# Kernel optimization log

Hardware: AMD Instinct MI355X
Metric: run time of the kernel (lower is better)

Reference implementation:

```python
import jax, jax.numpy as jnp
import numpy as np

B, S, HID = 1, 2048, 2304
H, KV, D = 8, 4, 256
FF = 9216
CAP = 50.0                      # attn_logit_softcapping
SCALE = 256.0 ** -0.5           # query_pre_attn_scalar ** -0.5
WIN = 1024                      # sliding_window_size
EPS = 1e-6
NEG = -2.3819763e38


def setup_inputs() -> dict:
    key = jax.random.key(0)
    ks = jax.random.split(key, 11)
    w = lambda k, shp: jax.random.normal(k, shp, jnp.float32) * 0.02
    ln = lambda k: jax.random.normal(k, (HID,), jnp.float32) * 0.1
    hidden_states = jax.random.normal(ks[0], (B, S, HID), jnp.float32)
    qkv_w = w(ks[1], (HID, (H + 2 * KV) * D))
    o_w = w(ks[2], (H * D, HID))
    gate_w = w(ks[3], (HID, FF))
    up_w = w(ks[4], (HID, FF))
    down_w = w(ks[5], (FF, HID))
    in_ln_w = ln(ks[6]); post_attn_ln_w = ln(ks[7])
    pre_ffw_ln_w = ln(ks[8]); post_ffw_ln_w = ln(ks[9])
    # precompute_freqs_cis (theta=10000) as cos/sin of shape [S, D//2]
    inv = 1.0 / (10000.0 ** (np.arange(0, D, 2)[: D // 2].astype(np.float64) / D))
    fr = np.outer(np.arange(S), inv)
    cos = jnp.asarray(np.cos(fr), jnp.float32)
    sin = jnp.asarray(np.sin(fr), jnp.float32)
    kv_write_indices = jnp.arange(S, dtype=jnp.int32)
    k_cache = jnp.zeros((B, S, KV, D), jnp.float32)
    v_cache = jnp.zeros((B, S, KV, D), jnp.float32)
    causal = jnp.tril(jnp.ones((S, S), bool))
    mask = jnp.where(causal, 0.0, NEG).astype(jnp.float32)[None, None]
    return dict(hidden_states=hidden_states, qkv_w=qkv_w, o_w=o_w,
                gate_w=gate_w, up_w=up_w, down_w=down_w,
                in_ln_w=in_ln_w, post_attn_ln_w=post_attn_ln_w,
                pre_ffw_ln_w=pre_ffw_ln_w, post_ffw_ln_w=post_ffw_ln_w,
                cos=cos, sin=sin, kv_write_indices=kv_write_indices,
                k_cache=k_cache, v_cache=v_cache, mask=mask)


def rmsnorm(x, wt):
    x = x.astype(jnp.float32)
    x = x * jax.lax.rsqrt(jnp.mean(x * x, axis=-1, keepdims=True) + EPS)
    return x * (1.0 + wt)  # add_unit_offset=True


def rope(x, cos, sin):
    # x: [b,s,h,d]; complex rotation with real=first half, imag=second half
    x1, x2 = jnp.split(x, 2, axis=-1)
    c = cos[None, :, None, :]
    s = sin[None, :, None, :]
    return jnp.concatenate([x1 * c - x2 * s, x1 * s + x2 * c], axis=-1)


def reference(hidden_states, qkv_w, o_w, gate_w, up_w, down_w,
              in_ln_w, post_attn_ln_w, pre_ffw_ln_w, post_ffw_ln_w,
              cos, sin, kv_write_indices, k_cache, v_cache, mask):
    residual = hidden_states
    x = rmsnorm(hidden_states, in_ln_w)
    qkv = x @ qkv_w
    q = qkv[..., : H * D].reshape(B, S, H, D)
    k = qkv[..., H * D: H * D + KV * D].reshape(B, S, KV, D)
    v = qkv[..., H * D + KV * D:].reshape(B, S, KV, D)
    q = rope(q, cos, sin)
    k = rope(k, cos, sin)
    kc = k_cache.at[:, kv_write_indices].set(k)
    vc = v_cache.at[:, kv_write_indices].set(v)
    g = H // KV
    kr = jnp.repeat(kc, g, axis=2)   # GQA repeat_interleave -> [B,S,H,D]
    vr = jnp.repeat(vc, g, axis=2)
    scores = jnp.einsum('bqhd,bkhd->bhqk', q * SCALE, kr)
    pos = jnp.arange(S)
    band = jnp.abs(pos[:, None] - pos[None, :]) <= (WIN - 1)
    m = jnp.where(band[None, None], mask, NEG)
    scores = jnp.tanh(scores / CAP) * CAP + m
    probs = jax.nn.softmax(scores.astype(jnp.float32), axis=-1)
    attn = jnp.einsum('bhqk,bkhd->bqhd', probs, vr).reshape(B, S, H * D)
    attn = attn @ o_w
    h = residual + rmsnorm(attn, post_attn_ln_w)
    residual = h
    x = rmsnorm(h, pre_ffw_ln_w)
    x = jax.nn.gelu(x @ gate_w, approximate=True) * (x @ up_w)
    x = x @ down_w
    x = rmsnorm(x, post_ffw_ln_w)
    return residual + x
```

## Files before the change

kernel.cpp:

```cpp
#include <hip/hip_runtime.h>
#include <hip/hip_bf16.h>
#include <cstdint>
#include <cstddef>

#define S_LEN  2048
#define HIDDEN 2304
#define NHEAD  8
#define NKVH   4
#define DHEAD  256
#define FFDIM  9216
#define QKVN   4096
#define ODIM   2048
#define WINM1  1023
#define QSCALE 0.0625f
#define CAPF   50.0f
#define PSTR   ((size_t)S_LEN * HIDDEN)

typedef __attribute__((ext_vector_type(4))) float f32x4;
typedef __attribute__((ext_vector_type(8))) short s16x8;

__device__ __forceinline__ void gload_lds16(const void* gptr, void* lptr) {
  __builtin_amdgcn_global_load_lds(
      (const __attribute__((address_space(1))) unsigned int*)gptr,
      (__attribute__((address_space(3))) unsigned int*)lptr, 16, 0, 0);
}

__global__ void k_fill(float* p, float v, size_t n) {
  size_t i = (size_t)blockIdx.x * blockDim.x + threadIdx.x;
  size_t st = (size_t)gridDim.x * blockDim.x;
  for (; i < n; i += st) p[i] = v;
}

__global__ void k_transpose_bf16(const float* __restrict__ in, __hip_bfloat16* __restrict__ out,
                                 int R, int C) {
  __shared__ float tile[32][33];
  const int c0 = blockIdx.x * 32, r0 = blockIdx.y * 32;
  const int tc = threadIdx.x & 31, tr = threadIdx.x >> 5;
#pragma unroll
  for (int i = 0; i < 4; i++)
    tile[tr + 8 * i][tc] = in[(size_t)(r0 + tr + 8 * i) * C + c0 + tc];
  __syncthreads();
#pragma unroll
  for (int i = 0; i < 4; i++)
    out[(size_t)(c0 + tr + 8 * i) * R + r0 + tc] = __float2bfloat16(tile[tc][tr + 8 * i]);
}

template <int NP, bool INBF16, bool ADD, bool BF16OUT>
__global__ void k_rmsnorm(const void* __restrict__ xv, const float* __restrict__ w,
                          const float* __restrict__ res, void* __restrict__ outv) {
  const int row = blockIdx.x;
  __shared__ float xs[HIDDEN];
  float ss = 0.f;
  for (int i = threadIdx.x; i < HIDDEN; i += 256) {
    float v = 0.f;
#pragma unroll
    for (int p = 0; p < NP; p++) {
      if constexpr (INBF16)
        v += __bfloat162float(((const __hip_bfloat16*)xv)[(size_t)p * PSTR + (size_t)row * HIDDEN + i]);
      else
        v += ((const float*)xv)[(size_t)p * PSTR + (size_t)row * HIDDEN + i];
    }
    xs[i] = v;
    ss += v * v;
  }
#pragma unroll
  for (int off = 32; off >= 1; off >>= 1) ss += __shfl_down(ss, off);
  __shared__ float red[4];
  __shared__ float srstd;
  if ((threadIdx.x & 63) == 0) red[threadIdx.x >> 6] = ss;
  __syncthreads();
  if (threadIdx.x == 0) {
    float tot = red[0] + red[1] + red[2] + red[3];
    srstd = rsqrtf(tot / (float)HIDDEN + 1e-6f);
  }
  __syncthreads();
  const float rstd = srstd;
  for (int i = threadIdx.x; i < HIDDEN; i += 256) {
    float v = xs[i] * rstd * (1.f + w[i]);
    if constexpr (ADD) v += res[(size_t)row * HIDDEN + i];
    if constexpr (BF16OUT)
      ((__hip_bfloat16*)outv)[(size_t)row * HIDDEN + i] = __float2bfloat16(v);
    else
      ((float*)outv)[(size_t)row * HIDDEN + i] = v;
  }
}

__global__ void k_rmsnorm2(const float* __restrict__ planes, const float* __restrict__ w1,
                           const float* __restrict__ res, const float* __restrict__ w2,
                           float* __restrict__ hf, __hip_bfloat16* __restrict__ xb) {
  const int row = blockIdx.x;
  __shared__ float xs[HIDDEN];
  __shared__ float red[4];
  __shared__ float srstd;
  float ss = 0.f;
  for (int i = threadIdx.x; i < HIDDEN; i += 256) {
    const float v = planes[(size_t)row * HIDDEN + i] + planes[PSTR + (size_t)row * HIDDEN + i];
    xs[i] = v;
    ss += v * v;
  }
#pragma unroll
  for (int off = 32; off >= 1; off >>= 1) ss += __shfl_down(ss, off);
  if ((threadIdx.x & 63) == 0) red[threadIdx.x >> 6] = ss;
  __syncthreads();
  if (threadIdx.x == 0)
    srstd = rsqrtf((red[0] + red[1] + red[2] + red[3]) / (float)HIDDEN + 1e-6f);
  __syncthreads();
  const float rstd1 = srstd;
  float ss2 = 0.f;
  for (int i = threadIdx.x; i < HIDDEN; i += 256) {
    const float h = res[(size_t)row * HIDDEN + i] + xs[i] * rstd1 * (1.f + w1[i]);
    hf[(size_t)row * HIDDEN + i] = h;
    ss2 += h * h;
  }
  __syncthreads();
  for (int i = threadIdx.x; i < HIDDEN; i += 256)
    xs[i] = hf[(size_t)row * HIDDEN + i];
#pragma unroll
  for (int off = 32; off >= 1; off >>= 1) ss2 += __shfl_down(ss2, off);
  if ((threadIdx.x & 63) == 0) red[threadIdx.x >> 6] = ss2;
  __syncthreads();
  if (threadIdx.x == 0)
    srstd = rsqrtf((red[0] + red[1] + red[2] + red[3]) / (float)HIDDEN + 1e-6f);
  __syncthreads();
  const float rstd2 = srstd;
  for (int i = threadIdx.x; i < HIDDEN; i += 256)
    xb[(size_t)row * HIDDEN + i] = __float2bfloat16(xs[i] * rstd2 * (1.f + w2[i]));
}

template <int EPI>
__global__ __launch_bounds__(256) void k_gemm_bt(const __hip_bfloat16* __restrict__ A,
                                                 const __hip_bfloat16* __restrict__ Bt,
                                                 void* __restrict__ Cv,
                                                 const __hip_bfloat16* __restrict__ G,
                                                 int N, int K) {
  __shared__ alignas(16) __hip_bfloat16 sA[128 * 64];
  __shared__ alignas(16) __hip_bfloat16 sB[128 * 64];
  const int t = threadIdx.x;
  const int w = t >> 6;
  const int wm = w >> 1, wn = w & 1;
  const int nwg = gridDim.x * gridDim.y;
  const int fblk = blockIdx.y * gridDim.x + blockIdx.x;
  const int qq = nwg >> 3, r8 = nwg & 7;
  const int xcd = fblk & 7, ix = fblk >> 3;
  const int swz = (xcd < r8 ? xcd * (qq + 1) : r8 * (qq + 1) + (xcd - r8) * qq) + ix;
  const int m0 = (swz % gridDim.y) * 128, n0 = (swz / gridDim.y) * 128;
  const int lr = t & 15, lg = (t & 63) >> 4;
  const int srow = t >> 3, sc8 = t & 7;

  f32x4 acc[4][4];
#pragma unroll
  for (int a = 0; a < 4; a++)
#pragma unroll
    for (int b = 0; b < 4; b++) acc[a][b] = (f32x4){0.f, 0.f, 0.f, 0.f};

  for (int kt = 0; kt < K; kt += 64) {
#pragma unroll
    for (int i = 0; i < 4; i++) {
      const __hip_bfloat16* g = A + (size_t)(m0 + i * 32 + srow) * K + kt + sc8 * 8;
      gload_lds16(g, sA + (size_t)(i * 256 + w * 64) * 8);
    }
#pragma unroll
    for (int i = 0; i < 4; i++) {
      const __hip_bfloat16* g = Bt + (size_t)(n0 + i * 32 + srow) * K + kt + sc8 * 8;
      gload_lds16(g, sB + (size_t)(i * 256 + w * 64) * 8);
    }
    __syncthreads();
#pragma unroll
    for (int ks = 0; ks < 2; ks++) {
      s16x8 af[4], bfr[4];
#pragma unroll
      for (int fm = 0; fm < 4; fm++)
        af[fm] = *reinterpret_cast<const s16x8*>(sA + (wm * 64 + fm * 16 + lr) * 64 + ks * 32 + lg * 8);
#pragma unroll
      for (int fn = 0; fn < 4; fn++)
        bfr[fn] = *reinterpret_cast<const s16x8*>(sB + (wn * 64 + fn * 16 + lr) * 64 + ks * 32 + lg * 8);
#pragma unroll
      for (int fm = 0; fm < 4; fm++)
#pragma unroll
        for (int fn = 0; fn < 4; fn++)
          acc[fm][fn] = __builtin_amdgcn_mfma_f32_16x16x32_bf16(af[fm], bfr[fn], acc[fm][fn], 0, 0, 0);
    }
    __syncthreads();
  }
#pragma unroll
  for (int fm = 0; fm < 4; fm++) {
    const int rb = m0 + wm * 64 + fm * 16 + lg * 4;
#pragma unroll
    for (int fn = 0; fn < 4; fn++) {
      const int col = n0 + wn * 64 + fn * 16 + lr;
#pragma unroll
      for (int j = 0; j < 4; j++) {
        const size_t idx = (size_t)(rb + j) * N + col;
        if constexpr (EPI == 0) {
          ((float*)Cv)[idx] = acc[fm][fn][j];
        } else if constexpr (EPI == 1) {
          ((__hip_bfloat16*)Cv)[idx] = __float2bfloat16(acc[fm][fn][j]);
        } else {
          const float x = __bfloat162float(G[idx]);
          const float tt = tanhf(0.7978845608028654f * (x + 0.044715f * x * x * x));
          ((__hip_bfloat16*)Cv)[idx] = __float2bfloat16(0.5f * x * (1.f + tt) * acc[fm][fn][j]);
        }
      }
    }
  }
}

template <int EPI>
__global__ __launch_bounds__(512, 2) void k_gemm8(const __hip_bfloat16* __restrict__ A,
                                                  const __hip_bfloat16* __restrict__ Bt,
                                                  void* __restrict__ Cv,
                                                  const __hip_bfloat16* __restrict__ G,
                                                  const __hip_bfloat16* __restrict__ Bt2,
                                                  void* __restrict__ Cv2,
                                                  int N, int K, int keff) {
  __shared__ alignas(16) __hip_bfloat16 smem[65536];
  const int t = threadIdx.x;
  const int w = t >> 6;
  const int wm = w >> 2, wn = w & 3;
  const int l = t & 63;
  const int lr = l & 15, lg = l >> 4;

  const int nxy = gridDim.x * gridDim.y;
  const int nwg = nxy * gridDim.z;
  const int fblk = blockIdx.z * nxy + blockIdx.y * gridDim.x + blockIdx.x;
  const int qq = nwg >> 3, r8 = nwg & 7;
  const int xcd = fblk & 7, ix = fblk >> 3;
  const int swz = (xcd < r8 ? xcd * (qq + 1) : r8 * (qq + 1) + (xcd - r8) * qq) + ix;
  const int plane = swz / nxy;
  const int rem = swz % nxy;
  const int m0 = (rem % gridDim.y) * 256, n0 = (rem / gridDim.y) * 256;
  const int k0 = plane * keff;

  const __hip_bfloat16* Bsrc = Bt;
  int nb0 = n0;
  if constexpr (EPI == 3) {
    if (n0 >= FFDIM) { Bsrc = Bt2; nb0 = n0 - FFDIM; }
  }

  const int sA8 = l & 7;
  size_t aoff[2], boff[2];
#pragma unroll
  for (int j = 0; j < 2; j++) {
    const int rv = (w * 2 + j) * 8 + (l >> 3);
    const int ko = (sA8 ^ (rv & 7)) * 8;
    aoff[j] = (size_t)(m0 + ((rv >> 6) & 1) * 128 + ((rv >> 4) & 3) * 16 + (rv & 15)) * K + k0 + ko;
    boff[j] = (size_t)(nb0 + ((rv >> 5) & 3) * 64 + ((rv >> 4) & 1) * 16 + (rv & 15)) * K + k0 + ko;
  }
  const int sl0 = ((lg) ^ (lr & 7)) * 8;
  const int sl1 = ((4 + lg) ^ (lr & 7)) * 8;

  f32x4 acc[8][4];
#pragma unroll
  for (int a = 0; a < 8; a++)
#pragma unroll
    for (int b = 0; b < 4; b++) acc[a][b] = (f32x4){0.f, 0.f, 0.f, 0.f};
  s16x8 af[4][2], bfr[2][2][2];

#define STG_A(bu, h, kti) { _Pragma("unroll") for (int j = 0; j < 2; j++) \
    gload_lds16(A + aoff[j] + (size_t)(h) * 64 * K + (size_t)(kti) * 64, \
                smem + (bu) * 32768 + (h) * 8192 + (w * 2 + j) * 512); }
#define STG_B(bu, h, kti) { _Pragma("unroll") for (int j = 0; j < 2; j++) \
    gload_lds16(Bsrc + boff[j] + (size_t)(h) * 32 * K + (size_t)(kti) * 64, \
                smem + (bu) * 32768 + 16384 + (h) * 8192 + (w * 2 + j) * 512); }
#define RD_A(bu, fmh) { const __hip_bfloat16* ab_ = smem + (bu) * 32768; \
    _Pragma("unroll") for (int f2 = 0; f2 < 4; f2++) { \
      const int ro_ = ((fmh) * 128 + wm * 64 + f2 * 16 + lr) * 64; \
      af[f2][0] = *(const s16x8*)(ab_ + ro_ + sl0); \
      af[f2][1] = *(const s16x8*)(ab_ + ro_ + sl1); } }
#define RD_BH(bu, fnh) { const __hip_bfloat16* bb_ = smem + (bu) * 32768 + 16384; \
    _Pragma("unroll") for (int f2 = 0; f2 < 2; f2++) { \
      const int ro_ = ((fnh) * 128 + wn * 32 + f2 * 16 + lr) * 64; \
      bfr[fnh][f2][0] = *(const s16x8*)(bb_ + ro_ + sl0); \
      bfr[fnh][f2][1] = *(const s16x8*)(bb_ + ro_ + sl1); } }
#define MFMA16(fmh, fnh) { __builtin_amdgcn_s_setprio(1); \
    _Pragma("unroll") for (int f2 = 0; f2 < 4; f2++) \
    _Pragma("unroll") for (int g2 = 0; g2 < 2; g2++) \
    _Pragma("unroll") for (int ks = 0; ks < 2; ks++) \
      acc[(fmh) * 4 + f2][(fnh) * 2 + g2] = __builtin_amdgcn_mfma_f32_16x16x32_bf16( \
          af[f2][ks], bfr[fnh][g2][ks], acc[(fmh) * 4 + f2][(fnh) * 2 + g2], 0, 0, 0); \
    __builtin_amdgcn_s_setprio(0); }
#define BARR() asm volatile("s_barrier" ::: "memory")
#define LGKM0() asm volatile("s_waitcnt lgkmcnt(0)" ::: "memory")
#define VMC4() asm volatile("s_waitcnt vmcnt(4)" ::: "memory")
#define VMC0() asm volatile("s_waitcnt vmcnt(0)" ::: "memory")

  STG_A(0, 0, 0); STG_A(0, 1, 0); STG_B(0, 0, 0); STG_B(0, 1, 0);
  STG_A(1, 0, 1); STG_A(1, 1, 1);
  VMC4(); BARR();

  const int niter = keff >> 7;
  for (int i = 0; i < niter; ++i) {
    const int t1 = 2 * i + 1;
    const bool more = (i + 1 < niter);
    RD_A(0, 0); RD_BH(0, 0);
    STG_B(1, 0, t1);
    BARR(); LGKM0(); MFMA16(0, 0); BARR();
    RD_BH(0, 1);
    STG_B(1, 1, t1);
    if (more) STG_A(0, 0, t1 + 1);
    BARR(); LGKM0(); MFMA16(0, 1); BARR();
    RD_A(0, 1);
    BARR(); LGKM0(); MFMA16(1, 0); BARR();
    if (more) STG_A(0, 1, t1 + 1);
    BARR(); LGKM0(); MFMA16(1, 1);
    if (more) { VMC4(); } else { VMC0(); }
    BARR();
    RD_A(1, 0); RD_BH(1, 0);
    if (more) STG_B(0, 0, t1 + 1);
    BARR(); LGKM0(); MFMA16(0, 0); BARR();
    RD_BH(1, 1);
    if (more) STG_B(0, 1, t1 + 1);
    BARR(); LGKM0(); MFMA16(0, 1); BARR();
    RD_A(1, 1);
    if (more) STG_A(1, 0, t1 + 2);
    BARR(); LGKM0(); MFMA16(1, 0); BARR();
    if (more) STG_A(1, 1, t1 + 2);
    BARR(); LGKM0(); MFMA16(1, 1);
    if (more) { VMC4(); }
    BARR();
  }
#undef STG_A
#undef STG_B
#undef RD_A
#undef RD_BH
#undef MFMA16
#undef BARR
#undef LGKM0
#undef VMC4
#undef VMC0

  __hip_bfloat16* Cw = nullptr;
  int cbase = n0, cstride = N;
  if constexpr (EPI == 3) {
    Cw = (__hip_bfloat16*)((n0 < FFDIM) ? Cv : Cv2);
    cbase = (n0 < FFDIM) ? n0 : n0 - FFDIM;
    cstride = FFDIM;
  }
#pragma unroll
  for (int fm = 0; fm < 8; fm++) {
    const int rb = m0 + wm * 128 + fm * 16 + lg * 4;
#pragma unroll
    for (int fn = 0; fn < 4; fn++) {
      const int coln = wn * 64 + fn * 16 + lr;
#pragma unroll
      for (int j = 0; j < 4; j++) {
        if constexpr (EPI == 3) {
          Cw[(size_t)(rb + j) * cstride + cbase + coln] = __float2bfloat16(acc[fm][fn][j]);
        } else {
          const size_t idxo = (size_t)(rb + j) * N + n0 + coln;
          if constexpr (EPI == 0) {
            ((float*)Cv)[idxo] = acc[fm][fn][j];
          } else if constexpr (EPI == 1) {
            ((__hip_bfloat16*)Cv)[idxo] = __float2bfloat16(acc[fm][fn][j]);
          } else if constexpr (EPI == 2) {
            const float x = __bfloat162float(G[idxo]);
            const float tg = tanhf(0.7978845608028654f * (x + 0.044715f * x * x * x));
            ((__hip_bfloat16*)Cv)[idxo] = __float2bfloat16(0.5f * x * (1.f + tg) * acc[fm][fn][j]);
          } else if constexpr (EPI == 4) {
            float* P = (plane == 0) ? (float*)Cv : (float*)Cv2;
            P[idxo] = acc[fm][fn][j];
          } else {
            ((__hip_bfloat16*)Cv)[(size_t)plane * PSTR + idxo] = __float2bfloat16(acc[fm][fn][j]);
          }
        }
      }
    }
  }
}

__global__ void k_gelu_mul2(const __hip_bfloat16* __restrict__ g, const __hip_bfloat16* __restrict__ u,
                            __hip_bfloat16* __restrict__ o, int n8) {
  const int st = gridDim.x * blockDim.x;
  for (int i = blockIdx.x * blockDim.x + threadIdx.x; i < n8; i += st) {
    s16x8 gv = *(const s16x8*)(g + (size_t)i * 8);
    s16x8 uv = *(const s16x8*)(u + (size_t)i * 8);
    s16x8 ov;
#pragma unroll
    for (int j = 0; j < 8; j++) {
      const float x = __uint_as_float(((uint32_t)(uint16_t)gv[j]) << 16);
      const float uu = __uint_as_float(((uint32_t)(uint16_t)uv[j]) << 16);
      const float tt = tanhf(0.7978845608028654f * (x + 0.044715f * x * x * x));
      const float r = 0.5f * x * (1.f + tt) * uu;
      ov[j] = (short)(__hip_bfloat16_raw(__float2bfloat16(r)).x);
    }
    *(s16x8*)(o + (size_t)i * 8) = ov;
  }
}

__global__ void k_rope_split(const float* __restrict__ p0, const float* __restrict__ p1,
                             const float* __restrict__ cosb, const float* __restrict__ sinb,
                             __hip_bfloat16* __restrict__ qo, __hip_bfloat16* __restrict__ ko) {
  const int s = blockIdx.x;
  const float* r0 = p0 + (size_t)s * QKVN;
  const float* r1 = p1 + (size_t)s * QKVN;
  const float* cr = cosb + (size_t)s * 128;
  const float* sr = sinb + (size_t)s * 128;
  for (int idx = threadIdx.x; idx < (NHEAD + NKVH) * 128; idx += 256) {
    const int hh = idx >> 7, d = idx & 127;
    const float cv = cr[d], sv = sr[d];
    if (hh < NHEAD) {
      const float x1 = r0[hh * DHEAD + d] + r1[hh * DHEAD + d];
      const float x2 = r0[hh * DHEAD + 128 + d] + r1[hh * DHEAD + 128 + d];
      const size_t base = ((size_t)hh * S_LEN + s) * DHEAD;
      qo[base + d]       = __float2bfloat16((x1 * cv - x2 * sv) * QSCALE);
      qo[base + 128 + d] = __float2bfloat16((x1 * sv + x2 * cv) * QSCALE);
    } else {
      const int kv = hh - NHEAD;
      const int o1 = NHEAD * DHEAD + kv * DHEAD + d;
      const float x1 = r0[o1] + r1[o1];
      const float x2 = r0[o1 + 128] + r1[o1 + 128];
      const size_t base = ((size_t)kv * S_LEN + s) * DHEAD;
      ko[base + d]       = __float2bfloat16(x1 * cv - x2 * sv);
      ko[base + 128 + d] = __float2bfloat16(x1 * sv + x2 * cv);
    }
  }
}

__global__ __launch_bounds__(256) void k_vsplit_t(const float* __restrict__ p0,
                                                  const float* __restrict__ p1,
                                                  __hip_bfloat16* __restrict__ vt) {
  __shared__ float tile[64][260];
  const int s0 = blockIdx.x * 64, kv = blockIdx.y;
  const int t = threadIdx.x;
  const int rr = t >> 6, c4 = t & 63;
#pragma unroll
  for (int p = 0; p < 16; p++) {
    const int row = rr + p * 4;
    const size_t go = (size_t)(s0 + row) * QKVN + (NHEAD + NKVH) * DHEAD + kv * DHEAD + c4 * 4;
    const float4 v0 = *(const float4*)(p0 + go);
    const float4 v1 = *(const float4*)(p1 + go);
    float4 v;
    v.x = v0.x + v1.x; v.y = v0.y + v1.y; v.z = v0.z + v1.z; v.w = v0.w + v1.w;
    *(float4*)(&tile[row][c4 * 4]) = v;
  }
  __syncthreads();
  const int c = t & 31, dr = t >> 5;
#pragma unroll
  for (int p = 0; p < 32; p++) {
    const int d = dr + p * 8;
    __hip_bfloat162 pr;
    pr.x = __float2bfloat16(tile[2 * c][d]);
    pr.y = __float2bfloat16(tile[2 * c + 1][d]);
    *(__hip_bfloat162*)(vt + ((size_t)kv * DHEAD + d) * S_LEN + s0 + 2 * c) = pr;
  }
}

__global__ __launch_bounds__(256) void k_attn_mfma(const __hip_bfloat16* __restrict__ Q,
                                                   const __hip_bfloat16* __restrict__ Kb,
                                                   const __hip_bfloat16* __restrict__ Vt,
                                                   __hip_bfloat16* __restrict__ O) {
  __shared__ alignas(16) __hip_bfloat16 Ks[64 * 264];
  __shared__ alignas(16) __hip_bfloat16 Vs[256 * 72];
  __shared__ alignas(16) __hip_bfloat16 Ps[64 * 72];
  const int h = blockIdx.y, kvh = h >> 1;
  const int q0 = blockIdx.x * 64;
  const int t = threadIdx.x;
  const int wq = t >> 6;
  const int l = t & 63;
  const int lr = l & 15, lg = l >> 4;

  s16x8 qf[8];
  {
    const __hip_bfloat16* qrow = Q + ((size_t)h * S_LEN + q0 + wq * 16 + lr) * DHEAD;
#pragma unroll
    for (int ks = 0; ks < 8; ks++) qf[ks] = *(const s16x8*)(qrow + ks * 32 + lg * 8);
  }
  f32x4 acc[16];
#pragma unroll
  for (int i = 0; i < 16; i++) acc[i] = (f32x4){0.f, 0.f, 0.f, 0.f};
  float rsum[4] = {0.f, 0.f, 0.f, 0.f};

  int lo = q0 - WINM1;
  if (lo < 0) lo = 0;
  lo &= ~63;
  const int qrow_base = q0 + wq * 16 + lg * 4;

  for (int kc = lo; kc <= q0; kc += 64) {
#pragma unroll
    for (int p = 0; p < 8; p++) {
      const int idx = t + p * 256;
      const int row = idx >> 5, c16 = idx & 31;
      s16x8 v = *(const s16x8*)(Kb + ((size_t)kvh * S_LEN + kc + row) * DHEAD + c16 * 8);
      *(s16x8*)(Ks + row * 264 + c16 * 8) = v;
    }
#pragma unroll
    for (int p = 0; p < 8; p++) {
      const int idx = t + p * 256;
      const int d = idx >> 3, ch = idx & 7;
      s16x8 v = *(const s16x8*)(Vt + ((size_t)kvh * DHEAD + d) * S_LEN + kc + ch * 8);
      *(s16x8*)(Vs + d * 72 + ch * 8) = v;
    }
    __syncthreads();

    f32x4 sc[4];
#pragma unroll
    for (int fq = 0; fq < 4; fq++) {
      sc[fq] = (f32x4){0.f, 0.f, 0.f, 0.f};
#pragma unroll
      for (int ks = 0; ks < 8; ks++) {
        s16x8 bfr = *(const s16x8*)(Ks + (fq * 16 + lr) * 264 + ks * 32 + lg * 8);
        sc[fq] = __builtin_amdgcn_mfma_f32_16x16x32_bf16(qf[ks], bfr, sc[fq], 0, 0, 0);
      }
    }
#pragma unroll
    for (int fq = 0; fq < 4; fq++) {
      const int k = kc + fq * 16 + lr;
#pragma unroll
      for (int j = 0; j < 4; j++) {
        const int qw = qrow_base + j;
        float p = 0.f;
        if (k <= qw && qw - k <= WINM1) {
          const float s = sc[fq][j];
          const float u = exp2f(s * 0.057707801635558534f);
          const float arg = 72.134752044448169f -
                            144.26950408889634f * __builtin_amdgcn_rcpf(u + 1.f);
          p = exp2f(arg);
        }
        const __hip_bfloat16 pb = __float2bfloat16(p);
        Ps[(wq * 16 + lg * 4 + j) * 72 + fq * 16 + lr] = pb;
        rsum[j] += __bfloat162float(pb);
      }
    }
#pragma unroll
    for (int ks2 = 0; ks2 < 2; ks2++) {
      s16x8 pa = *(const s16x8*)(Ps + (wq * 16 + lr) * 72 + ks2 * 32 + lg * 8);
#pragma unroll
      for (int f2 = 0; f2 < 16; f2++) {
        s16x8 vb = *(const s16x8*)(Vs + (f2 * 16 + lr) * 72 + ks2 * 32 + lg * 8);
        acc[f2] = __builtin_amdgcn_mfma_f32_16x16x32_bf16(pa, vb, acc[f2], 0, 0, 0);
      }
    }
    __syncthreads();
  }
#pragma unroll
  for (int j = 0; j < 4; j++) {
    float s = rsum[j];
#pragma unroll
    for (int off = 1; off < 16; off <<= 1) s += __shfl_xor(s, off, 64);
    rsum[j] = 1.f / s;
  }
#pragma unroll
  for (int f2 = 0; f2 < 16; f2++)
#pragma unroll
    for (int j = 0; j < 4; j++)
      O[(size_t)(qrow_base + j) * ODIM + h * DHEAD + f2 * 16 + lr] =
          __float2bfloat16(acc[f2][j] * rsum[j]);
}

extern "C" void kernel_launch(void* const* d_in, const int* in_sizes, int n_in,
                              void* d_out, int out_size, void* d_ws, size_t ws_size,
                              hipStream_t stream) {
  const float* hidden  = (const float*)d_in[0];
  const float* qkv_w   = (const float*)d_in[1];
  const float* o_w     = (const float*)d_in[2];
  const float* gate_w  = (const float*)d_in[3];
  const float* up_w    = (const float*)d_in[4];
  const float* down_w  = (const float*)d_in[5];
  const float* in_ln   = (const float*)d_in[6];
  const float* post_attn_ln = (const float*)d_in[7];
  const float* pre_ffw_ln   = (const float*)d_in[8];
  const float* post_ffw_ln  = (const float*)d_in[9];
  const float* cosb    = (const float*)d_in[10];
  const float* sinb    = (const float*)d_in[11];
  float* out = (float*)d_out;
  char* ws = (char*)d_ws;

  const size_t OFF_W   = 0;
  const size_t OFF_HF  = 42467328;
  const size_t OFF_X   = 61341696;
  const size_t OFF_S1  = 70778880;
  const size_t OFF_S2  = 108527616;
  const size_t NEED    = 146276352;
  const size_t OFF_W2  = 146276352;
  const size_t NEED_F  = 188743680;

  if (ws_size < NEED) {
    k_fill<<<1024, 256, 0, stream>>>(out, 100000.0f + (float)(ws_size >> 20), (size_t)out_size);
    return;
  }
  const bool FUSED = (ws_size >= NEED_F);

  __hip_bfloat16* W    = (__hip_bfloat16*)(ws + OFF_W);
  __hip_bfloat16* W2   = (__hip_bfloat16*)(ws + OFF_W2);
  float*          Hf   = (float*)(ws + OFF_HF);
  __hip_bfloat16* Xb   = (__hip_bfloat16*)(ws + OFF_X);
  __hip_bfloat16* GATEB= (__hip_bfloat16*)(ws + OFF_S1);
  __hip_bfloat16* UPB  = (__hip_bfloat16*)(ws + OFF_S2);
  __hip_bfloat16* Qb   = (__hip_bfloat16*)(ws + OFF_S2);
  __hip_bfloat16* Kb   = (__hip_bfloat16*)(ws + OFF_S2 + 8388608);
  __hip_bfloat16* Vtb  = (__hip_bfloat16*)(ws + OFF_S2 + 12582912);
  __hip_bfloat16* ATTN = (__hip_bfloat16*)(ws + OFF_S2 + 29360128);

  if (FUSED) {
    float* QKV0 = (float*)(ws + OFF_S1);
    float* QKV1 = (float*)(ws + OFF_W2);
    float* PROJ = (float*)(ws + OFF_S1);
    __hip_bfloat16* DPART = (__hip_bfloat16*)(ws + OFF_S2);

    k_transpose_bf16<<<dim3(QKVN / 32, HIDDEN / 32), 256, 0, stream>>>(qkv_w, W, HIDDEN, QKVN);
    k_rmsnorm<1, false, false, true><<<S_LEN, 256, 0, stream>>>(hidden, in_ln, nullptr, Xb);
    k_gemm8<4><<<dim3(QKVN / 256, S_LEN / 256, 2), 512, 0, stream>>>(
        Xb, W, QKV0, nullptr, nullptr, QKV1, QKVN, HIDDEN, HIDDEN / 2);
    k_rope_split<<<S_LEN, 256, 0, stream>>>(QKV0, QKV1, cosb, sinb, Qb, Kb);
    k_vsplit_t<<<dim3(S_LEN / 64, NKVH), 256, 0, stream>>>(QKV0, QKV1, Vtb);
    k_attn_mfma<<<dim3(S_LEN / 64, NHEAD), 256, 0, stream>>>(Qb, Kb, Vtb, ATTN);
    k_transpose_bf16<<<dim3(HIDDEN / 32, ODIM / 32), 256, 0, stream>>>(o_w, W, ODIM, HIDDEN);
    k_gemm8<4><<<dim3(HIDDEN / 256, S_LEN / 256, 2), 512, 0, stream>>>(
        ATTN, W, PROJ, nullptr, nullptr, PROJ + PSTR, HIDDEN, ODIM, ODIM / 2);
    k_rmsnorm2<<<S_LEN, 256, 0, stream>>>(PROJ, post_attn_ln, hidden, pre_ffw_ln, Hf, Xb);
    k_transpose_bf16<<<dim3(FFDIM / 32, HIDDEN / 32), 256, 0, stream>>>(gate_w, W, HIDDEN, FFDIM);
    k_transpose_bf16<<<dim3(FFDIM / 32, HIDDEN / 32), 256, 0, stream>>>(up_w, W2, HIDDEN, FFDIM);
    k_gemm8<3><<<dim3((2 * FFDIM) / 256, S_LEN / 256, 1), 512, 0, stream>>>(
        Xb, W, GATEB, nullptr, W2, UPB, FFDIM, HIDDEN, HIDDEN);
    k_gelu_mul2<<<2048, 256, 0, stream>>>(GATEB, UPB, GATEB, (S_LEN * FFDIM) / 8);
    k_transpose_bf16<<<dim3(HIDDEN / 32, FFDIM / 32), 256, 0, stream>>>(down_w, W, FFDIM, HIDDEN);
    k_gemm8<5><<<dim3(HIDDEN / 256, S_LEN / 256, 8), 512, 0, stream>>>(
        GATEB, W, DPART, nullptr, nullptr, nullptr, HIDDEN, FFDIM, FFDIM / 8);
    k_rmsnorm<8, true, true, false><<<S_LEN, 256, 0, stream>>>(DPART, post_ffw_ln, Hf, out);
  } else {
    float* QKV = (float*)(ws + OFF_S1);
    float* PROJ = (float*)(ws + OFF_S2);
    k_transpose_bf16<<<dim3(QKVN / 32, HIDDEN / 32), 256, 0, stream>>>(qkv_w, W, HIDDEN, QKVN);
    k_rmsnorm<1, false, false, true><<<S_LEN, 256, 0, stream>>>(hidden, in_ln, nullptr, Xb);
    k_gemm_bt<0><<<dim3(QKVN / 128, S_LEN / 128), 256, 0, stream>>>(Xb, W, QKV, nullptr, QKVN, HIDDEN);
    k_fill<<<1024, 256, 0, stream>>>(Hf, 0.f, PSTR);
    k_rope_split<<<S_LEN, 256, 0, stream>>>(QKV, Hf, cosb, sinb, Qb, Kb);
    k_vsplit_t<<<dim3(S_LEN / 64, NKVH), 256, 0, stream>>>(QKV, Hf, Vtb);
    k_attn_mfma<<<dim3(S_LEN / 64, NHEAD), 256, 0, stream>>>(Qb, Kb, Vtb, ATTN);
    k_transpose_bf16<<<dim3(HIDDEN / 32, ODIM / 32), 256, 0, stream>>>(o_w, W, ODIM, HIDDEN);
    k_gemm_bt<0><<<dim3(HIDDEN / 128, S_LEN / 128), 256, 0, stream>>>(ATTN, W, PROJ, nullptr, HIDDEN, ODIM);
    k_rmsnorm<1, false, true, false><<<S_LEN, 256, 0, stream>>>(PROJ, post_attn_ln, hidden, Hf);
    k_rmsnorm<1, false, false, true><<<S_LEN, 256, 0, stream>>>(Hf, pre_ffw_ln, nullptr, Xb);
    k_transpose_bf16<<<dim3(FFDIM / 32, HIDDEN / 32), 256, 0, stream>>>(gate_w, W, HIDDEN, FFDIM);
    k_gemm_bt<1><<<dim3(FFDIM / 128, S_LEN / 128), 256, 0, stream>>>(Xb, W, GATEB, nullptr, FFDIM, HIDDEN);
    __hip_bfloat16* ACT = (__hip_bfloat16*)(ws + OFF_S2);
    k_transpose_bf16<<<dim3(FFDIM / 32, HIDDEN / 32), 256, 0, stream>>>(up_w, W, HIDDEN, FFDIM);
    k_gemm_bt<2><<<dim3(FFDIM / 128, S_LEN / 128), 256, 0, stream>>>(Xb, W, ACT, GATEB, FFDIM, HIDDEN);
    float* Yf = (float*)(ws + OFF_S1);
    k_transpose_bf16<<<dim3(HIDDEN / 32, FFDIM / 32), 256, 0, stream>>>(down_w, W, FFDIM, HIDDEN);
    k_gemm_bt<0><<<dim3(HIDDEN / 128, S_LEN / 128), 256, 0, stream>>>(ACT, W, Yf, nullptr, HIDDEN, FFDIM);
    k_rmsnorm<1, false, true, false><<<S_LEN, 256, 0, stream>>>(Yf, post_ffw_ln, Hf, out);
  }
}
```

Measured before the change: 682.9 us.

## Add 256x192-tile GEMM kernel for hidden-dimension and FFN projections

```diff
diff --git a/kernel.cpp b/kernel.cpp
--- a/kernel.cpp
+++ b/kernel.cpp
@@ -231,12 +231,6 @@
   const int m0 = (rem % gridDim.y) * 256, n0 = (rem / gridDim.y) * 256;
   const int k0 = plane * keff;
 
-  const __hip_bfloat16* Bsrc = Bt;
-  int nb0 = n0;
-  if constexpr (EPI == 3) {
-    if (n0 >= FFDIM) { Bsrc = Bt2; nb0 = n0 - FFDIM; }
-  }
-
   const int sA8 = l & 7;
   size_t aoff[2], boff[2];
 #pragma unroll
@@ -244,7 +238,7 @@
     const int rv = (w * 2 + j) * 8 + (l >> 3);
     const int ko = (sA8 ^ (rv & 7)) * 8;
     aoff[j] = (size_t)(m0 + ((rv >> 6) & 1) * 128 + ((rv >> 4) & 3) * 16 + (rv & 15)) * K + k0 + ko;
-    boff[j] = (size_t)(nb0 + ((rv >> 5) & 3) * 64 + ((rv >> 4) & 1) * 16 + (rv & 15)) * K + k0 + ko;
+    boff[j] = (size_t)(n0 + ((rv >> 5) & 3) * 64 + ((rv >> 4) & 1) * 16 + (rv & 15)) * K + k0 + ko;
   }
   const int sl0 = ((lg) ^ (lr & 7)) * 8;
   const int sl1 = ((4 + lg) ^ (lr & 7)) * 8;
@@ -260,7 +254,7 @@
     gload_lds16(A + aoff[j] + (size_t)(h) * 64 * K + (size_t)(kti) * 64, \
                 smem + (bu) * 32768 + (h) * 8192 + (w * 2 + j) * 512); }
 #define STG_B(bu, h, kti) { _Pragma("unroll") for (int j = 0; j < 2; j++) \
-    gload_lds16(Bsrc + boff[j] + (size_t)(h) * 32 * K + (size_t)(kti) * 64, \
+    gload_lds16(Bt + boff[j] + (size_t)(h) * 32 * K + (size_t)(kti) * 64, \
                 smem + (bu) * 32768 + 16384 + (h) * 8192 + (w * 2 + j) * 512); }
 #define RD_A(bu, fmh) { const __hip_bfloat16* ab_ = smem + (bu) * 32768; \
     _Pragma("unroll") for (int f2 = 0; f2 < 4; f2++) { \
@@ -329,6 +323,161 @@
 #undef VMC4
 #undef VMC0
 
+#pragma unroll
+  for (int fm = 0; fm < 8; fm++) {
+    const int rb = m0 + wm * 128 + fm * 16 + lg * 4;
+#pragma unroll
+    for (int fn = 0; fn < 4; fn++) {
+      const int coln = wn * 64 + fn * 16 + lr;
+#pragma unroll
+      for (int j = 0; j < 4; j++) {
+        const size_t idxo = (size_t)(rb + j) * N + n0 + coln;
+        if constexpr (EPI == 4) {
+          float* P = (plane == 0) ? (float*)Cv : (float*)Cv2;
+          P[idxo] = acc[fm][fn][j];
+        } else {
+          ((__hip_bfloat16*)Cv)[idxo] = __float2bfloat16(acc[fm][fn][j]);
+        }
+      }
+    }
+  }
+}
+
+template <int EPI>
+__global__ __launch_bounds__(512, 2) void k_gemm192(const __hip_bfloat16* __restrict__ A,
+                                                    const __hip_bfloat16* __restrict__ Bt,
+                                                    void* __restrict__ Cv,
+                                                    const __hip_bfloat16* __restrict__ Bt2,
+                                                    void* __restrict__ Cv2,
+                                                    int N, int K, int keff) {
+  __shared__ alignas(16) __hip_bfloat16 smem[57344];
+  const int t = threadIdx.x;
+  const int w = t >> 6;
+  const int wm = w >> 2, wn = w & 3;
+  const int l = t & 63;
+  const int lr = l & 15, lg = l >> 4;
+
+  const int nxy = gridDim.x * gridDim.y;
+  const int nwg = nxy * gridDim.z;
+  const int fblk = blockIdx.z * nxy + blockIdx.y * gridDim.x + blockIdx.x;
+  const int qq = nwg >> 3, r8 = nwg & 7;
+  const int xcd = fblk & 7, ix = fblk >> 3;
+  const int swz = (xcd < r8 ? xcd * (qq + 1) : r8 * (qq + 1) + (xcd - r8) * qq) + ix;
+  const int plane = swz / nxy;
+  const int rem = swz % nxy;
+  const int m0 = (rem % gridDim.y) * 256, n0 = (rem / gridDim.y) * 192;
+  const int k0 = plane * keff;
+
+  const __hip_bfloat16* Bsrc = Bt;
+  int nb0 = n0;
+  if constexpr (EPI == 3) {
+    if (n0 >= FFDIM) { Bsrc = Bt2; nb0 = n0 - FFDIM; }
+  }
+
+  const int sA8 = l & 7;
+  size_t aoff[2];
+#pragma unroll
+  for (int j = 0; j < 2; j++) {
+    const int rv = (w * 2 + j) * 8 + (l >> 3);
+    const int ko = (sA8 ^ (rv & 7)) * 8;
+    aoff[j] = (size_t)(m0 + ((rv >> 6) & 1) * 128 + ((rv >> 4) & 3) * 16 + (rv & 15)) * K + k0 + ko;
+  }
+  const size_t boffh = (size_t)(nb0 + w * 8 + (l >> 3)) * K + k0 + ((sA8 ^ (l >> 3)) * 8);
+  const int sl0 = ((lg) ^ (lr & 7)) * 8;
+  const int sl1 = ((4 + lg) ^ (lr & 7)) * 8;
+
+  f32x4 acc[8][3];
+#pragma unroll
+  for (int a = 0; a < 8; a++)
+#pragma unroll
+    for (int b = 0; b < 3; b++) acc[a][b] = (f32x4){0.f, 0.f, 0.f, 0.f};
+  s16x8 af[4][2], bfr[3][2];
+
+#define GSTG_A(bu, h, kti) { _Pragma("unroll") for (int j = 0; j < 2; j++) \
+    gload_lds16(A + aoff[j] + (size_t)(h) * 64 * K + (size_t)(kti) * 64, \
+                smem + (bu) * 28672 + (h) * 8192 + (w * 2 + j) * 512); }
+#define GSTG_B(bu, c, kti) \
+    gload_lds16(Bsrc + boffh + (size_t)(c) * 64 * K + (size_t)(kti) * 64, \
+                smem + (bu) * 28672 + 16384 + ((c) * 64 + w * 8) * 64);
+#define GRD_A(bu, fmh) { const __hip_bfloat16* ab_ = smem + (bu) * 28672; \
+    _Pragma("unroll") for (int f2 = 0; f2 < 4; f2++) { \
+      const int ro_ = ((fmh) * 128 + wm * 64 + f2 * 16 + lr) * 64; \
+      af[f2][0] = *(const s16x8*)(ab_ + ro_ + sl0); \
+      af[f2][1] = *(const s16x8*)(ab_ + ro_ + sl1); } }
+#define GRD_B01(bu) { const __hip_bfloat16* bb_ = smem + (bu) * 28672 + 16384; \
+    _Pragma("unroll") for (int f2 = 0; f2 < 2; f2++) { \
+      const int ro_ = (wn * 48 + f2 * 16 + lr) * 64; \
+      bfr[f2][0] = *(const s16x8*)(bb_ + ro_ + sl0); \
+      bfr[f2][1] = *(const s16x8*)(bb_ + ro_ + sl1); } }
+#define GRD_B2(bu) { const __hip_bfloat16* bb_ = smem + (bu) * 28672 + 16384; \
+      const int ro_ = (wn * 48 + 32 + lr) * 64; \
+      bfr[2][0] = *(const s16x8*)(bb_ + ro_ + sl0); \
+      bfr[2][1] = *(const s16x8*)(bb_ + ro_ + sl1); }
+#define GMFMA01(fmh) { __builtin_amdgcn_s_setprio(1); \
+    _Pragma("unroll") for (int f2 = 0; f2 < 4; f2++) \
+    _Pragma("unroll") for (int g2 = 0; g2 < 2; g2++) \
+    _Pragma("unroll") for (int ks = 0; ks < 2; ks++) \
+      acc[(fmh) * 4 + f2][g2] = __builtin_amdgcn_mfma_f32_16x16x32_bf16( \
+          af[f2][ks], bfr[g2][ks], acc[(fmh) * 4 + f2][g2], 0, 0, 0); \
+    __builtin_amdgcn_s_setprio(0); }
+#define GMFMA2(fmh) { __builtin_amdgcn_s_setprio(1); \
+    _Pragma("unroll") for (int f2 = 0; f2 < 4; f2++) \
+    _Pragma("unroll") for (int ks = 0; ks < 2; ks++) \
+      acc[(fmh) * 4 + f2][2] = __builtin_amdgcn_mfma_f32_16x16x32_bf16( \
+          af[f2][ks], bfr[2][ks], acc[(fmh) * 4 + f2][2], 0, 0, 0); \
+    __builtin_amdgcn_s_setprio(0); }
+#define BARR() asm volatile("s_barrier" ::: "memory")
+#define LGKM0() asm volatile("s_waitcnt lgkmcnt(0)" ::: "memory")
+#define VMC4() asm volatile("s_waitcnt vmcnt(4)" ::: "memory")
+#define VMC0() asm volatile("s_waitcnt vmcnt(0)" ::: "memory")
+
+  GSTG_A(0, 0, 0); GSTG_A(0, 1, 0);
+  GSTG_B(0, 0, 0); GSTG_B(0, 1, 0); GSTG_B(0, 2, 0);
+  GSTG_A(1, 0, 1); GSTG_A(1, 1, 1);
+  VMC4(); BARR();
+
+  const int niter = keff >> 7;
+  for (int i = 0; i < niter; ++i) {
+    const int t1 = 2 * i + 1;
+    const bool more = (i + 1 < niter);
+    GRD_A(0, 0); GRD_B01(0);
+    GSTG_B(1, 0, t1); GSTG_B(1, 1, t1);
+    BARR(); LGKM0(); GMFMA01(0); BARR();
+    GRD_B2(0);
+    GSTG_B(1, 2, t1);
+    if (more) GSTG_A(0, 0, t1 + 1);
+    BARR(); LGKM0(); GMFMA2(0); BARR();
+    GRD_A(0, 1);
+    BARR(); LGKM0(); GMFMA01(1); BARR();
+    if (more) GSTG_A(0, 1, t1 + 1);
+    BARR(); LGKM0(); GMFMA2(1);
+    if (more) { VMC4(); } else { VMC0(); }
+    BARR();
+    GRD_A(1, 0); GRD_B01(1);
+    if (more) { GSTG_B(0, 0, t1 + 1); GSTG_B(0, 1, t1 + 1); }
+    BARR(); LGKM0(); GMFMA01(0); BARR();
+    GRD_B2(1);
+    if (more) { GSTG_B(0, 2, t1 + 1); GSTG_A(1, 0, t1 + 2); }
+    BARR(); LGKM0(); GMFMA2(0); BARR();
+    GRD_A(1, 1);
+    BARR(); LGKM0(); GMFMA01(1); BARR();
+    if (more) GSTG_A(1, 1, t1 + 2);
+    BARR(); LGKM0(); GMFMA2(1);
+    if (more) { VMC4(); }
+    BARR();
+  }
+#undef GSTG_A
+#undef GSTG_B
+#undef GRD_A
+#undef GRD_B01
+#undef GRD_B2
+#undef GMFMA01
+#undef GMFMA2
+#undef BARR
+#undef LGKM0
+#undef VMC4
+#undef VMC0
+
   __hip_bfloat16* Cw = nullptr;
   int cbase = n0, cstride = N;
   if constexpr (EPI == 3) {
@@ -340,28 +489,18 @@
   for (int fm = 0; fm < 8; fm++) {
     const int rb = m0 + wm * 128 + fm * 16 + lg * 4;
 #pragma unroll
-    for (int fn = 0; fn < 4; fn++) {
-      const int coln = wn * 64 + fn * 16 + lr;
+    for (int fn = 0; fn < 3; fn++) {
+      const int coln = wn * 48 + fn * 16 + lr;
 #pragma unroll
       for (int j = 0; j < 4; j++) {
         if constexpr (EPI == 3) {
           Cw[(size_t)(rb + j) * cstride + cbase + coln] = __float2bfloat16(acc[fm][fn][j]);
+        } else if constexpr (EPI == 4) {
+          float* P = (plane == 0) ? (float*)Cv : (float*)Cv2;
+          P[(size_t)(rb + j) * N + n0 + coln] = acc[fm][fn][j];
         } else {
-          const size_t idxo = (size_t)(rb + j) * N + n0 + coln;
-          if constexpr (EPI == 0) {
-            ((float*)Cv)[idxo] = acc[fm][fn][j];
-          } else if constexpr (EPI == 1) {
-            ((__hip_bfloat16*)Cv)[idxo] = __float2bfloat16(acc[fm][fn][j]);
-          } else if constexpr (EPI == 2) {
-            const float x = __bfloat162float(G[idxo]);
-            const float tg = tanhf(0.7978845608028654f * (x + 0.044715f * x * x * x));
-            ((__hip_bfloat16*)Cv)[idxo] = __float2bfloat16(0.5f * x * (1.f + tg) * acc[fm][fn][j]);
-          } else if constexpr (EPI == 4) {
-            float* P = (plane == 0) ? (float*)Cv : (float*)Cv2;
-            P[idxo] = acc[fm][fn][j];
-          } else {
-            ((__hip_bfloat16*)Cv)[(size_t)plane * PSTR + idxo] = __float2bfloat16(acc[fm][fn][j]);
-          }
+          ((__hip_bfloat16*)Cv)[(size_t)plane * PSTR + (size_t)(rb + j) * N + n0 + coln] =
+              __float2bfloat16(acc[fm][fn][j]);
         }
       }
     }
@@ -605,17 +744,17 @@
     k_vsplit_t<<<dim3(S_LEN / 64, NKVH), 256, 0, stream>>>(QKV0, QKV1, Vtb);
     k_attn_mfma<<<dim3(S_LEN / 64, NHEAD), 256, 0, stream>>>(Qb, Kb, Vtb, ATTN);
     k_transpose_bf16<<<dim3(HIDDEN / 32, ODIM / 32), 256, 0, stream>>>(o_w, W, ODIM, HIDDEN);
-    k_gemm8<4><<<dim3(HIDDEN / 256, S_LEN / 256, 2), 512, 0, stream>>>(
-        ATTN, W, PROJ, nullptr, nullptr, PROJ + PSTR, HIDDEN, ODIM, ODIM / 2);
+    k_gemm192<4><<<dim3(HIDDEN / 192, S_LEN / 256, 2), 512, 0, stream>>>(
+        ATTN, W, PROJ, nullptr, PROJ + PSTR, HIDDEN, ODIM, ODIM / 2);
     k_rmsnorm2<<<S_LEN, 256, 0, stream>>>(PROJ, post_attn_ln, hidden, pre_ffw_ln, Hf, Xb);
     k_transpose_bf16<<<dim3(FFDIM / 32, HIDDEN / 32), 256, 0, stream>>>(gate_w, W, HIDDEN, FFDIM);
     k_transpose_bf16<<<dim3(FFDIM / 32, HIDDEN / 32), 256, 0, stream>>>(up_w, W2, HIDDEN, FFDIM);
-    k_gemm8<3><<<dim3((2 * FFDIM) / 256, S_LEN / 256, 1), 512, 0, stream>>>(
-        Xb, W, GATEB, nullptr, W2, UPB, FFDIM, HIDDEN, HIDDEN);
+    k_gemm192<3><<<dim3((2 * FFDIM) / 192, S_LEN / 256, 1), 512, 0, stream>>>(
+        Xb, W, GATEB, W2, UPB, FFDIM, HIDDEN, HIDDEN);
     k_gelu_mul2<<<2048, 256, 0, stream>>>(GATEB, UPB, GATEB, (S_LEN * FFDIM) / 8);
     k_transpose_bf16<<<dim3(HIDDEN / 32, FFDIM / 32), 256, 0, stream>>>(down_w, W, FFDIM, HIDDEN);
-    k_gemm8<5><<<dim3(HIDDEN / 256, S_LEN / 256, 8), 512, 0, stream>>>(
-        GATEB, W, DPART, nullptr, nullptr, nullptr, HIDDEN, FFDIM, FFDIM / 8);
+    k_gemm192<5><<<dim3(HIDDEN / 192, S_LEN / 256, 8), 512, 0, stream>>>(
+        GATEB, W, DPART, nullptr, nullptr, HIDDEN, FFDIM, FFDIM / 8);
     k_rmsnorm<8, true, true, false><<<S_LEN, 256, 0, stream>>>(DPART, post_ffw_ln, Hf, out);
   } else {
     float* QKV = (float*)(ws + OFF_S1);
```

After: 647.7 us. -5.2%, faster.
